# Performance work log

Measured on AMD Instinct MI355X. Metric: run time of the kernel, lower is better.

## Reference

```python
import jax, jax.numpy as jnp
import numpy as np

B, S, D, H = 2, 2048, 1024, 16
DK = D // H


def setup_inputs() -> dict:
    key = jax.random.key(0)
    ks = jax.random.split(key, 12)
    s = 0.02
    return {
        "q": jax.random.normal(ks[0], (B, S, D), jnp.float32),
        "k": jax.random.normal(ks[1], (B, S, D), jnp.float32),
        "v": jax.random.normal(ks[2], (B, S, D), jnp.float32),
        "mask": jax.random.randint(ks[3], (1, 1, S, S), 0, 2, jnp.int32),
        "Wq": jax.random.normal(ks[4], (D, D), jnp.float32) * s,
        "bq": jnp.zeros((D,), jnp.float32),
        "Wk": jax.random.normal(ks[5], (D, D), jnp.float32) * s,
        "bk": jnp.zeros((D,), jnp.float32),
        "Wv": jax.random.normal(ks[6], (D, D), jnp.float32) * s,
        "bv": jnp.zeros((D,), jnp.float32),
        "Wo": jax.random.normal(ks[7], (D, D), jnp.float32) * s,
        "bo": jnp.zeros((D,), jnp.float32),
    }


def reference(q, k, v, mask, Wq, bq, Wk, bk, Wv, bv, Wo, bo):
    # linear projections (torch Linear: x @ W.T + b)
    qp = q @ Wq.T + bq
    kp = k @ Wk.T + bk
    vp = v @ Wv.T + bv
    # [B, S, D] -> [B, H, S, DK]
    split = lambda x: x.reshape(B, S, H, DK).transpose(0, 2, 1, 3)
    qh, kh, vh = split(qp), split(kp), split(vp)
    scale = 1.0 / jnp.sqrt(jnp.float32(DK))
    attn = jnp.einsum('bhsd,bhtd->bhst', qh, kh) * scale  # [B,H,S,S]
    attn = jnp.where(mask == 0, jnp.float32(-1e9), attn)
    attn = jax.nn.softmax(attn, axis=-1)
    out = jnp.einsum('bhst,bhtd->bhsd', attn, vh)  # [B,H,S,DK]
    concat = out.transpose(0, 2, 1, 3).reshape(B, S, D)
    return concat @ Wo.T + bo
```

## Files before the change

kernel.cpp:

```cpp
#include <hip/hip_runtime.h>
#include <hip/hip_bf16.h>


using bf16x8 = __attribute__((ext_vector_type(8))) short;
using f32x4  = __attribute__((ext_vector_type(4))) float;

constexpr int Bc = 2, Sc = 2048, Dc = 1024, Hc = 16, DKc = 64;
constexpr int Mc = Bc * Sc;
#define QSCALE 0.18033688011112042f

__device__ __forceinline__ void lds_load16(const void* g, void* l) {
  __builtin_amdgcn_global_load_lds(
      (const __attribute__((address_space(1))) unsigned int*)g,
      (__attribute__((address_space(3))) unsigned int*)l, 16, 0, 0);
}

#if __has_builtin(__builtin_amdgcn_exp2f)
__device__ __forceinline__ float exp2_fast(float x) { return __builtin_amdgcn_exp2f(x); }
#else
__device__ __forceinline__ float exp2_fast(float x) {
  float r;
  asm("v_exp_f32 %0, %1\n\ts_nop 0" : "=v"(r) : "v"(x));
  return r;
}
#endif

__device__ __forceinline__ unsigned pack_trunc(float a, float b) {
  return __builtin_amdgcn_perm(__float_as_uint(b), __float_as_uint(a), 0x07060302u);
}

__device__ __forceinline__ unsigned pack2bf(float a, float b) {
  union { __hip_bfloat16 h; unsigned short s; } ua, ub;
  ua.h = __float2bfloat16(a);
  ub.h = __float2bfloat16(b);
  return (unsigned)ua.s | ((unsigned)ub.s << 16);
}

__global__ void prep(const float* __restrict__ q, const float* __restrict__ k,
                     const float* __restrict__ v, const int* __restrict__ mask,
                     const float* __restrict__ Wq, const float* __restrict__ Wk,
                     const float* __restrict__ Wv, const float* __restrict__ Wo,
                     char* __restrict__ ws) {
  const size_t MB = 1024 * 1024;
  int blk = blockIdx.x;
  if (blk < 12288) {
    int which = blk >> 12;
    int i = (((blk & 4095) << 8) + threadIdx.x) * 4;
    const float* s = which == 0 ? q : (which == 1 ? k : v);
    __hip_bfloat16* d = (__hip_bfloat16*)(ws + (size_t)which * 8 * MB);
    float4 x = *(const float4*)&s[i];
    uint2 pk = {pack2bf(x.x, x.y), pack2bf(x.z, x.w)};
    *(uint2*)&d[i] = pk;
  } else if (blk < 16384) {
    int bb = blk - 12288;
    int which = bb >> 10;
    int i = (((bb & 1023) << 8) + threadIdx.x) * 4;
    const float* s = which == 0 ? Wq : (which == 1 ? Wk : (which == 2 ? Wv : Wo));
    __hip_bfloat16* d = which < 3 ? (__hip_bfloat16*)(ws + (24 + 2 * which) * MB)
                                  : (__hip_bfloat16*)(ws + 30 * MB);
    float4 x = *(const float4*)&s[i];
    uint2 pk = {pack2bf(x.x, x.y), pack2bf(x.z, x.w)};
    *(uint2*)&d[i] = pk;
  } else {
    int i = ((blk - 16384) << 8) + threadIdx.x;
    unsigned long long bal = __ballot(mask[i] != 0);
    if ((threadIdx.x & 63) == 0)
      ((unsigned long long*)(ws + 32 * MB))[i >> 6] = bal;
  }
}

__global__ __launch_bounds__(256, 3) void proj_qkv(
    const __hip_bfloat16* __restrict__ qb, const __hip_bfloat16* __restrict__ kb,
    const __hip_bfloat16* __restrict__ vb, const __hip_bfloat16* __restrict__ Wcat,
    const float* __restrict__ bq, const float* __restrict__ bk,
    const float* __restrict__ bv, __hip_bfloat16* __restrict__ qhd,
    __hip_bfloat16* __restrict__ khd, __hip_bfloat16* __restrict__ vtd) {
  __shared__ __align__(16) __hip_bfloat16 As[2][128 * 32];
  __shared__ __align__(16) __hip_bfloat16 Bs[2][128 * 32];
  const int tid = threadIdx.x;
  const int f = blockIdx.x, g = f >> 3;
  const int m0 = ((f & 7) * 4 + g / 24) * 128;
  const int n0 = (g % 24) * 128;
  const int which = n0 >> 10, nl0 = n0 & 1023;
  const __hip_bfloat16* X = which == 0 ? qb : (which == 1 ? kb : vb);
  const float* bias = which == 0 ? bq : (which == 1 ? bk : bv);
  const int w = tid >> 6, lane = tid & 63, ln = lane & 15, quad = lane >> 4;
  const int rl = w * 32 + (lane >> 2);
  const int sw8 = ((lane & 3) ^ ((lane >> 2) & 3)) * 8;
  const int aoff = (n0 + rl) * 1024 + sw8;
  const int boff = (m0 + rl) * 1024 + sw8;
  char* aDst = (char*)As + w * 2048 + lane * 16;
  char* bDst = (char*)Bs + w * 2048 + lane * 16;
  const int rkq = (quad ^ (ln & 3)) * 16;
  const int rA0 = ((w >> 1) * 64 + ln) * 64 + rkq;
  const int rB0 = ((w & 1) * 64 + ln) * 64 + rkq;
  f32x4 acc[4][4] = {};

#define PSTAGE(KO, BI)                                                        \
  {                                                                           \
    lds_load16(&Wcat[aoff + (KO)], aDst + (BI)*8192);                         \
    lds_load16(&Wcat[aoff + 16384 + (KO)], aDst + (BI)*8192 + 1024);          \
    lds_load16(&X[boff + (KO)], bDst + (BI)*8192);                            \
    lds_load16(&X[boff + 16384 + (KO)], bDst + (BI)*8192 + 1024);             \
  }

  PSTAGE(0, 0);
  if (which == 2) {
    for (int kb32 = 0; kb32 < 32; ++kb32) {
      const int bi = kb32 & 1;
      __syncthreads();
      if (kb32 < 31) PSTAGE((kb32 + 1) * 32, bi ^ 1);
      bf16x8 af[4], bf[4];
#pragma unroll
      for (int i = 0; i < 4; ++i)
        af[i] = *(bf16x8*)((char*)As + bi * 8192 + rA0 + i * 1024);
#pragma unroll
      for (int j = 0; j < 4; ++j)
        bf[j] = *(bf16x8*)((char*)Bs + bi * 8192 + rB0 + j * 1024);
#pragma unroll
      for (int i = 0; i < 4; ++i)
#pragma unroll
        for (int j = 0; j < 4; ++j)
          acc[i][j] = __builtin_amdgcn_mfma_f32_16x16x32_bf16(bf[j], af[i],
                                                              acc[i][j], 0, 0, 0);
    }
  } else {
    for (int kb32 = 0; kb32 < 32; ++kb32) {
      const int bi = kb32 & 1;
      __syncthreads();
      if (kb32 < 31) PSTAGE((kb32 + 1) * 32, bi ^ 1);
      bf16x8 af[4], bf[4];
#pragma unroll
      for (int i = 0; i < 4; ++i)
        af[i] = *(bf16x8*)((char*)As + bi * 8192 + rA0 + i * 1024);
#pragma unroll
      for (int j = 0; j < 4; ++j)
        bf[j] = *(bf16x8*)((char*)Bs + bi * 8192 + rB0 + j * 1024);
#pragma unroll
      for (int i = 0; i < 4; ++i)
#pragma unroll
        for (int j = 0; j < 4; ++j)
          acc[i][j] = __builtin_amdgcn_mfma_f32_16x16x32_bf16(af[i], bf[j],
                                                              acc[i][j], 0, 0, 0);
    }
  }

  const int wA = (w >> 1) * 64, wB = (w & 1) * 64;
  if (which == 2) {
#pragma unroll
    for (int i = 0; i < 4; ++i) {
      int nf = nl0 + wA + i * 16 + ln;
      int h = nf >> 6, dk = nf & 63;
      float bb = bias[nf];
#pragma unroll
      for (int j = 0; j < 4; ++j) {
        int sb = m0 + wB + j * 16 + quad * 4;
        int b = sb >> 11, s = sb & 2047;
        float vv[4] = {acc[i][j][0] + bb, acc[i][j][1] + bb,
                       acc[i][j][2] + bb, acc[i][j][3] + bb};
        uint2 pk = {pack2bf(vv[0], vv[1]), pack2bf(vv[2], vv[3])};
        *(uint2*)&vtd[(((size_t)(b * Hc + h) * DKc + dk) * Sc) + s] = pk;
      }
    }
  } else {
#pragma unroll
    for (int i = 0; i < 4; ++i) {
      int nfb = nl0 + wA + i * 16 + quad * 4;
      float4 b4 = *(const float4*)&bias[nfb];
      int h = nfb >> 6, dk0 = nfb & 63;
#pragma unroll
      for (int j = 0; j < 4; ++j) {
        int sg = m0 + wB + j * 16 + ln;
        int b = sg >> 11, s = sg & 2047;
        float vv[4] = {acc[i][j][0] + b4.x, acc[i][j][1] + b4.y,
                       acc[i][j][2] + b4.z, acc[i][j][3] + b4.w};
        if (which == 0) {
          uint2 pk = {pack2bf(vv[0] * QSCALE, vv[1] * QSCALE),
                      pack2bf(vv[2] * QSCALE, vv[3] * QSCALE)};
          *(uint2*)&qhd[(((size_t)(b * Hc + h) * Sc + s) * DKc) + dk0] = pk;
        } else {
          uint2 pk = {pack2bf(vv[0], vv[1]), pack2bf(vv[2], vv[3])};
          *(uint2*)&khd[(((size_t)(b * Hc + h) * Sc + s) * DKc) + dk0] = pk;
        }
      }
    }
  }
}

__global__ __launch_bounds__(256, 2) void gemm_out(
    const __hip_bfloat16* __restrict__ X, const __hip_bfloat16* __restrict__ W,
    const float* __restrict__ bias, float* __restrict__ Y) {
  __shared__ __align__(16) __hip_bfloat16 As[2][64 * 64];
  __shared__ __align__(16) __hip_bfloat16 Bs[2][128 * 64];
  const int tid = threadIdx.x;
  const int f = blockIdx.x, g = f >> 3;
  const int m0 = ((f & 7) * 4 + (g >> 4)) * 128;
  const int n0 = (g & 15) * 64;
  const int w = tid >> 6, lane = tid & 63, ln = lane & 15, quad = lane >> 4;
  const int wA = (w & 1) * 32, wB = (w >> 1) * 64;
  const int swz = ((lane & 7) ^ (lane >> 3)) * 8;
  const int rk0 = ln * 128 + ((quad ^ (ln & 7)) * 16);
  const int rk1 = ln * 128 + (((quad + 4) ^ (ln & 7)) * 16);
  const int aoff = (n0 + w * 16 + (lane >> 3)) * 1024 + swz;
  const int boff = (m0 + w * 32 + (lane >> 3)) * 1024 + swz;
  f32x4 acc[2][4] = {};

#define OSTAGE(KO, BI)                                                        \
  {                                                                           \
    _Pragma("unroll") for (int i = 0; i < 2; ++i)                             \
        lds_load16(&W[aoff + i * 8192 + (KO)],                                \
                   (char*)As[BI] + w * 2048 + lane * 16 + i * 1024);          \
    _Pragma("unroll") for (int i = 0; i < 4; ++i)                             \
        lds_load16(&X[boff + i * 8192 + (KO)],                                \
                   (char*)Bs[BI] + w * 4096 + lane * 16 + i * 1024);          \
  }

  OSTAGE(0, 0);
  for (int kb64 = 0; kb64 < 16; ++kb64) {
    const int bi = kb64 & 1;
    __syncthreads();
    if (kb64 + 1 < 16) OSTAGE((kb64 + 1) * 64, bi ^ 1);
    bf16x8 af[2][2], bf[4][2];
#pragma unroll
    for (int i = 0; i < 2; ++i) {
      af[i][0] = *(bf16x8*)((char*)As[bi] + wA * 128 + i * 2048 + rk0);
      af[i][1] = *(bf16x8*)((char*)As[bi] + wA * 128 + i * 2048 + rk1);
    }
#pragma unroll
    for (int j = 0; j < 4; ++j) {
      bf[j][0] = *(bf16x8*)((char*)Bs[bi] + wB * 128 + j * 2048 + rk0);
      bf[j][1] = *(bf16x8*)((char*)Bs[bi] + wB * 128 + j * 2048 + rk1);
    }
#pragma unroll
    for (int i = 0; i < 2; ++i)
#pragma unroll
      for (int j = 0; j < 4; ++j) {
        acc[i][j] = __builtin_amdgcn_mfma_f32_16x16x32_bf16(af[i][0], bf[j][0],
                                                            acc[i][j], 0, 0, 0);
        acc[i][j] = __builtin_amdgcn_mfma_f32_16x16x32_bf16(af[i][1], bf[j][1],
                                                            acc[i][j], 0, 0, 0);
      }
  }
#pragma unroll
  for (int i = 0; i < 2; ++i) {
    int nfb = n0 + wA + i * 16 + quad * 4;
    float4 b4 = *(const float4*)&bias[nfb];
#pragma unroll
    for (int j = 0; j < 4; ++j) {
      int sg = m0 + wB + j * 16 + ln;
      float4 st = {acc[i][j][0] + b4.x, acc[i][j][1] + b4.y,
                   acc[i][j][2] + b4.z, acc[i][j][3] + b4.w};
      *(float4*)&Y[(size_t)sg * Dc + nfb] = st;
    }
  }
}

__global__ __launch_bounds__(256, 3) void flash_attn(
    const __hip_bfloat16* __restrict__ qh, const __hip_bfloat16* __restrict__ kh,
    const __hip_bfloat16* __restrict__ vt, const uint4* __restrict__ mb4,
    __hip_bfloat16* __restrict__ oc) {
  __shared__ __align__(16) char L[51200];
  const int tid = threadIdx.x;
  const int f = blockIdx.x, g = f >> 3;
  const int bh = (f & 7) * 4 + (g >> 4);
  const int q0 = (g & 15) * 128;
  const int b = bh >> 4, h = bh & 15;
  const int w = tid >> 6, lane = tid & 63, ln = lane & 15, quad = lane >> 4;
  const size_t base = (size_t)bh * Sc * DKc;
  const __hip_bfloat16* khb = kh + base;
  const __hip_bfloat16* vtb = vt + base;

  bf16x8 qf[2][2];
#pragma unroll
  for (int qt = 0; qt < 2; ++qt)
#pragma unroll
    for (int kc = 0; kc < 2; ++kc)
      qf[qt][kc] = *(const bf16x8*)&qh[base +
          (size_t)(q0 + w * 32 + qt * 16 + ln) * 64 + kc * 32 + quad * 8];

  bf16x8 onesA;
#pragma unroll
  for (int i = 0; i < 8; ++i) onesA[i] = (short)0x3F80;

  const int swz = ((lane & 7) ^ (lane >> 3)) * 8;
  const int rk0 = ln * 128 + ((quad ^ (ln & 7)) * 16);
  const int rk1 = ln * 128 + (((quad + 4) ^ (ln & 7)) * 16);
  const int rPw = 32768 + w * 4608 + ln * 144 + quad * 8;
  const int rPb = 32768 + w * 4608 + ln * 144 + quad * 16;
  char* dmaL = L + w * 2048 + lane * 16;
  int koff = (w * 16 + (lane >> 3)) * 64 + swz;
  int voff0 = (w * 16 + (lane >> 3)) * Sc + swz;
  int voff1 = voff0 + 8 * Sc;
  int midx0 = (q0 + w * 32 + ln) * 16;
  int midx1 = midx0 + 256;
  const int sh0 = quad * 4, sh1 = quad * 4 + 16;

#define KV_DMA(BI)                                                            \
  {                                                                           \
    lds_load16(khb + koff, dmaL + (BI)*8192);                                 \
    lds_load16(khb + koff + 512, dmaL + (BI)*8192 + 1024);                    \
    lds_load16(vtb + voff0, dmaL + 16384 + (BI)*8192);                        \
    lds_load16(vtb + voff1, dmaL + 16384 + (BI)*8192 + 1024);                 \
  }

  f32x4 Oacc[4][2] = {};
  f32x4 lacc[2] = {};
  KV_DMA(0);

#define FTILE(BUF, LO0, HI0, LO1, HI1)                                        \
  {                                                                           \
    bf16x8 kf[4][2];                                                          \
    _Pragma("unroll") for (int tt = 0; tt < 4; ++tt) {                        \
      kf[tt][0] = *(bf16x8*)(L + (BUF)*8192 + tt * 2048 + rk0);               \
      kf[tt][1] = *(bf16x8*)(L + (BUF)*8192 + tt * 2048 + rk1);               \
    }                                                                         \
    _Pragma("unroll") for (int qt = 0; qt < 2; ++qt) {                        \
      f32x4 s[4];                                                             \
      __builtin_amdgcn_s_setprio(1);                                          \
      _Pragma("unroll") for (int tt = 0; tt < 4; ++tt) {                      \
        f32x4 z = {0.f, 0.f, 0.f, 0.f};                                       \
        z = __builtin_amdgcn_mfma_f32_16x16x32_bf16(kf[tt][0], qf[qt][0], z,  \
                                                    0, 0, 0);                 \
        s[tt] = __builtin_amdgcn_mfma_f32_16x16x32_bf16(kf[tt][1], qf[qt][1], \
                                                        z, 0, 0, 0);          \
      }                                                                       \
      __builtin_amdgcn_s_setprio(0);                                          \
      unsigned lo = qt ? (LO1) : (LO0), hi = qt ? (HI1) : (HI0);              \
      _Pragma("unroll") for (int tt = 0; tt < 4; ++tt) {                      \
        unsigned word = (tt & 2) ? hi : lo;                                   \
        unsigned pre = word >> ((tt & 1) ? sh1 : sh0);                        \
        float p[4];                                                           \
        _Pragma("unroll") for (int r = 0; r < 4; ++r) {                       \
          float e = exp2_fast(s[tt][r]);                                      \
          p[r] = (pre & (1u << r)) ? e : 0.f;                                 \
        }                                                                     \
        uint2 pk = {pack_trunc(p[0], p[1]), pack_trunc(p[2], p[3])};          \
        *(uint2*)(L + rPw + qt * 2304 + tt * 32) = pk;                        \
      }                                                                       \
    }                                                                         \
    bf16x8 vf[4][2], pb[2][2];                                                \
    _Pragma("unroll") for (int dt = 0; dt < 4; ++dt) {                        \
      vf[dt][0] = *(bf16x8*)(L + 16384 + (BUF)*8192 + dt * 2048 + rk0);       \
      vf[dt][1] = *(bf16x8*)(L + 16384 + (BUF)*8192 + dt * 2048 + rk1);       \
    }                                                                         \
    _Pragma("unroll") for (int qt = 0; qt < 2; ++qt) {                        \
      pb[qt][0] = *(bf16x8*)(L + rPb + qt * 2304);                            \
      pb[qt][1] = *(bf16x8*)(L + rPb + qt * 2304 + 64);                       \
    }                                                                         \
    __builtin_amdgcn_s_setprio(1);                                            \
    _Pragma("unroll") for (int qt = 0; qt < 2; ++qt) {                        \
      lacc[qt] = __builtin_amdgcn_mfma_f32_16x16x32_bf16(onesA, pb[qt][0],    \
                                                         lacc[qt], 0, 0, 0);  \
      lacc[qt] = __builtin_amdgcn_mfma_f32_16x16x32_bf16(onesA, pb[qt][1],    \
                                                         lacc[qt], 0, 0, 0);  \
    }                                                                         \
    _Pragma("unroll") for (int dt = 0; dt < 4; ++dt)                          \
        _Pragma("unroll") for (int qt = 0; qt < 2; ++qt) {                    \
      Oacc[dt][qt] = __builtin_amdgcn_mfma_f32_16x16x32_bf16(                 \
          vf[dt][0], pb[qt][0], Oacc[dt][qt], 0, 0, 0);                       \
      Oacc[dt][qt] = __builtin_amdgcn_mfma_f32_16x16x32_bf16(                 \
          vf[dt][1], pb[qt][1], Oacc[dt][qt], 0, 0, 0);                       \
    }                                                                         \
    __builtin_amdgcn_s_setprio(0);                                            \
  }

  for (int it2 = 0; it2 < 16; ++it2) {
    __syncthreads();
    uint4 mq0 = mb4[midx0], mq1 = mb4[midx1];
    ++midx0; ++midx1;
    koff += 4096; voff0 += 64; voff1 += 64;
    KV_DMA(1);
    FTILE(0, mq0.x, mq0.y, mq1.x, mq1.y);
    __syncthreads();
    if (it2 < 15) {
      koff += 4096; voff0 += 64; voff1 += 64;
      KV_DMA(0);
    }
    FTILE(1, mq0.z, mq0.w, mq1.z, mq1.w);
  }

  float linv[2];
#pragma unroll
  for (int qt = 0; qt < 2; ++qt)
    linv[qt] = 1.f / fmaxf(lacc[qt][0], 1e-30f);
#pragma unroll
  for (int dt = 0; dt < 4; ++dt)
#pragma unroll
    for (int qt = 0; qt < 2; ++qt) {
      f32x4 o = Oacc[dt][qt];
      uint2 pk = {pack2bf(o[0] * linv[qt], o[1] * linv[qt]),
                  pack2bf(o[2] * linv[qt], o[3] * linv[qt])};
      *(uint2*)(L + rPw + qt * 2304 + dt * 32) = pk;
    }
  __builtin_amdgcn_s_waitcnt(0);
#pragma unroll
  for (int chunk = 0; chunk < 4; ++chunk) {
    int row = chunk * 8 + (lane >> 3);
    bf16x8 val = *(bf16x8*)(L + 32768 + w * 4608 + row * 144 + (lane & 7) * 16);
    int s = q0 + w * 32 + row;
    *(bf16x8*)&oc[(size_t)(b * Sc + s) * Dc + h * 64 + (lane & 7) * 8] = val;
  }
}

extern "C" void kernel_launch(void* const* d_in, const int* in_sizes, int n_in,
                              void* d_out, int out_size, void* d_ws, size_t ws_size,
                              hipStream_t stream) {
  const float* q  = (const float*)d_in[0];
  const float* k  = (const float*)d_in[1];
  const float* v  = (const float*)d_in[2];
  const int* mask = (const int*)d_in[3];
  const float* Wq = (const float*)d_in[4];
  const float* bq = (const float*)d_in[5];
  const float* Wk = (const float*)d_in[6];
  const float* bk = (const float*)d_in[7];
  const float* Wv = (const float*)d_in[8];
  const float* bv = (const float*)d_in[9];
  const float* Wo = (const float*)d_in[10];
  const float* bo = (const float*)d_in[11];

  char* ws = (char*)d_ws;
  const size_t MB = 1024 * 1024;
  __hip_bfloat16* qb   = (__hip_bfloat16*)(ws + 0 * MB);
  __hip_bfloat16* kb   = (__hip_bfloat16*)(ws + 8 * MB);
  __hip_bfloat16* vb   = (__hip_bfloat16*)(ws + 16 * MB);
  __hip_bfloat16* Wcat = (__hip_bfloat16*)(ws + 24 * MB);
  __hip_bfloat16* Wob  = (__hip_bfloat16*)(ws + 30 * MB);
  uint4*          mb4  = (uint4*)(ws + 32 * MB);
  __hip_bfloat16* qhd  = (__hip_bfloat16*)(ws + 33 * MB);
  __hip_bfloat16* khd  = (__hip_bfloat16*)(ws + 41 * MB);
  __hip_bfloat16* vtd  = (__hip_bfloat16*)(ws + 49 * MB);
  __hip_bfloat16* oc   = (__hip_bfloat16*)(ws + 57 * MB);

  prep<<<32768, 256, 0, stream>>>(q, k, v, mask, Wq, Wk, Wv, Wo, ws);
  proj_qkv<<<768, 256, 0, stream>>>(qb, kb, vb, Wcat, bq, bk, bv, qhd, khd, vtd);
  flash_attn<<<512, 256, 0, stream>>>(qhd, khd, vtd, mb4, oc);
  gemm_out<<<512, 256, 0, stream>>>(oc, Wob, bo, (float*)d_out);
}
```

Measured before the change: 241.4 us.

## Split flash-attention KV tiles across two wave groups with LDS reduction

Doubles the flash_attn block to 512 threads. Each pair of waves shares a 32-row query slice and splits every 64-key tile into two halves, so each wave does half the QK, softmax and PV work per tile. The partial O accumulators and row sums are combined through LDS at the end before the output is written. This raises per-CU wave parallelism to hide latency, at the cost of a final reduction, extra barriers, and tighter occupancy limits under launch_bounds(512,4).

```diff
diff --git a/kernel.cpp b/kernel.cpp
--- a/kernel.cpp
+++ b/kernel.cpp
@@ -255,7 +255,7 @@
   }
 }
 
-__global__ __launch_bounds__(256, 3) void flash_attn(
+__global__ __launch_bounds__(512, 4) void flash_attn(
     const __hip_bfloat16* __restrict__ qh, const __hip_bfloat16* __restrict__ kh,
     const __hip_bfloat16* __restrict__ vt, const uint4* __restrict__ mb4,
     __hip_bfloat16* __restrict__ oc) {
@@ -266,6 +266,7 @@
   const int q0 = (g & 15) * 128;
   const int b = bh >> 4, h = bh & 15;
   const int w = tid >> 6, lane = tid & 63, ln = lane & 15, quad = lane >> 4;
+  const int qg = w >> 1, kg = w & 1;
   const size_t base = (size_t)bh * Sc * DKc;
   const __hip_bfloat16* khb = kh + base;
   const __hip_bfloat16* vtb = vt + base;
@@ -276,7 +277,7 @@
 #pragma unroll
     for (int kc = 0; kc < 2; ++kc)
       qf[qt][kc] = *(const bf16x8*)&qh[base +
-          (size_t)(q0 + w * 32 + qt * 16 + ln) * 64 + kc * 32 + quad * 8];
+          (size_t)(q0 + qg * 32 + qt * 16 + ln) * 64 + kc * 32 + quad * 8];
 
   bf16x8 onesA;
 #pragma unroll
@@ -285,82 +286,69 @@
   const int swz = ((lane & 7) ^ (lane >> 3)) * 8;
   const int rk0 = ln * 128 + ((quad ^ (ln & 7)) * 16);
   const int rk1 = ln * 128 + (((quad + 4) ^ (ln & 7)) * 16);
-  const int rPw = 32768 + w * 4608 + ln * 144 + quad * 8;
-  const int rPb = 32768 + w * 4608 + ln * 144 + quad * 16;
-  char* dmaL = L + w * 2048 + lane * 16;
-  int koff = (w * 16 + (lane >> 3)) * 64 + swz;
-  int voff0 = (w * 16 + (lane >> 3)) * Sc + swz;
-  int voff1 = voff0 + 8 * Sc;
-  int midx0 = (q0 + w * 32 + ln) * 16;
+  const int rkv = ln * 128 + ((((kg << 2) + quad) ^ (ln & 7)) * 16);
+  const int rPw = 32768 + qg * 4608 + ln * 144 + kg * 64 + quad * 8;
+  const int rPb = 32768 + qg * 4608 + ln * 144 + kg * 64 + quad * 16;
+  char* dmaL = L + w * 1024 + lane * 16;
+  int koff = (w * 8 + (lane >> 3)) * 64 + swz;
+  int voff = (w * 8 + (lane >> 3)) * Sc + swz;
+  int midx0 = (q0 + qg * 32 + ln) * 16;
   int midx1 = midx0 + 256;
   const int sh0 = quad * 4, sh1 = quad * 4 + 16;
 
 #define KV_DMA(BI)                                                            \
   {                                                                           \
     lds_load16(khb + koff, dmaL + (BI)*8192);                                 \
-    lds_load16(khb + koff + 512, dmaL + (BI)*8192 + 1024);                    \
-    lds_load16(vtb + voff0, dmaL + 16384 + (BI)*8192);                        \
-    lds_load16(vtb + voff1, dmaL + 16384 + (BI)*8192 + 1024);                 \
+    lds_load16(vtb + voff, dmaL + 16384 + (BI)*8192);                         \
   }
 
   f32x4 Oacc[4][2] = {};
   f32x4 lacc[2] = {};
   KV_DMA(0);
 
-#define FTILE(BUF, LO0, HI0, LO1, HI1)                                        \
+#define FTILE(BUF, E0, E1)                                                    \
   {                                                                           \
-    bf16x8 kf[4][2];                                                          \
-    _Pragma("unroll") for (int tt = 0; tt < 4; ++tt) {                        \
-      kf[tt][0] = *(bf16x8*)(L + (BUF)*8192 + tt * 2048 + rk0);               \
-      kf[tt][1] = *(bf16x8*)(L + (BUF)*8192 + tt * 2048 + rk1);               \
+    bf16x8 kf[2][2];                                                          \
+    _Pragma("unroll") for (int tl = 0; tl < 2; ++tl) {                        \
+      kf[tl][0] = *(bf16x8*)(L + (BUF)*8192 + (kg * 2 + tl) * 2048 + rk0);    \
+      kf[tl][1] = *(bf16x8*)(L + (BUF)*8192 + (kg * 2 + tl) * 2048 + rk1);    \
     }                                                                         \
     _Pragma("unroll") for (int qt = 0; qt < 2; ++qt) {                        \
-      f32x4 s[4];                                                             \
+      f32x4 s4[2];                                                            \
       __builtin_amdgcn_s_setprio(1);                                          \
-      _Pragma("unroll") for (int tt = 0; tt < 4; ++tt) {                      \
+      _Pragma("unroll") for (int tl = 0; tl < 2; ++tl) {                      \
         f32x4 z = {0.f, 0.f, 0.f, 0.f};                                       \
-        z = __builtin_amdgcn_mfma_f32_16x16x32_bf16(kf[tt][0], qf[qt][0], z,  \
+        z = __builtin_amdgcn_mfma_f32_16x16x32_bf16(kf[tl][0], qf[qt][0], z,  \
                                                     0, 0, 0);                 \
-        s[tt] = __builtin_amdgcn_mfma_f32_16x16x32_bf16(kf[tt][1], qf[qt][1], \
-                                                        z, 0, 0, 0);          \
+        s4[tl] = __builtin_amdgcn_mfma_f32_16x16x32_bf16(kf[tl][1],           \
+                                                         qf[qt][1], z, 0, 0, 0); \
       }                                                                       \
       __builtin_amdgcn_s_setprio(0);                                          \
-      unsigned lo = qt ? (LO1) : (LO0), hi = qt ? (HI1) : (HI0);              \
-      _Pragma("unroll") for (int tt = 0; tt < 4; ++tt) {                      \
-        unsigned word = (tt & 2) ? hi : lo;                                   \
-        unsigned pre = word >> ((tt & 1) ? sh1 : sh0);                        \
+      unsigned word = qt ? (E1) : (E0);                                       \
+      _Pragma("unroll") for (int tl = 0; tl < 2; ++tl) {                      \
+        unsigned pre = word >> (tl ? sh1 : sh0);                              \
         float p[4];                                                           \
         _Pragma("unroll") for (int r = 0; r < 4; ++r) {                       \
-          float e = exp2_fast(s[tt][r]);                                      \
+          float e = exp2_fast(s4[tl][r]);                                     \
           p[r] = (pre & (1u << r)) ? e : 0.f;                                 \
         }                                                                     \
         uint2 pk = {pack_trunc(p[0], p[1]), pack_trunc(p[2], p[3])};          \
-        *(uint2*)(L + rPw + qt * 2304 + tt * 32) = pk;                        \
+        *(uint2*)(L + rPw + qt * 2304 + tl * 32) = pk;                        \
       }                                                                       \
     }                                                                         \
-    bf16x8 vf[4][2], pb[2][2];                                                \
-    _Pragma("unroll") for (int dt = 0; dt < 4; ++dt) {                        \
-      vf[dt][0] = *(bf16x8*)(L + 16384 + (BUF)*8192 + dt * 2048 + rk0);       \
-      vf[dt][1] = *(bf16x8*)(L + 16384 + (BUF)*8192 + dt * 2048 + rk1);       \
-    }                                                                         \
-    _Pragma("unroll") for (int qt = 0; qt < 2; ++qt) {                        \
-      pb[qt][0] = *(bf16x8*)(L + rPb + qt * 2304);                            \
-      pb[qt][1] = *(bf16x8*)(L + rPb + qt * 2304 + 64);                       \
-    }                                                                         \
+    bf16x8 vf[4], pb[2];                                                      \
+    _Pragma("unroll") for (int dt = 0; dt < 4; ++dt)                          \
+        vf[dt] = *(bf16x8*)(L + 16384 + (BUF)*8192 + dt * 2048 + rkv);        \
+    _Pragma("unroll") for (int qt = 0; qt < 2; ++qt)                          \
+        pb[qt] = *(bf16x8*)(L + rPb + qt * 2304);                             \
     __builtin_amdgcn_s_setprio(1);                                            \
-    _Pragma("unroll") for (int qt = 0; qt < 2; ++qt) {                        \
-      lacc[qt] = __builtin_amdgcn_mfma_f32_16x16x32_bf16(onesA, pb[qt][0],    \
-                                                         lacc[qt], 0, 0, 0);  \
-      lacc[qt] = __builtin_amdgcn_mfma_f32_16x16x32_bf16(onesA, pb[qt][1],    \
-                                                         lacc[qt], 0, 0, 0);  \
-    }                                                                         \
+    _Pragma("unroll") for (int qt = 0; qt < 2; ++qt)                          \
+        lacc[qt] = __builtin_amdgcn_mfma_f32_16x16x32_bf16(onesA, pb[qt],     \
+                                                           lacc[qt], 0, 0, 0); \
     _Pragma("unroll") for (int dt = 0; dt < 4; ++dt)                          \
-        _Pragma("unroll") for (int qt = 0; qt < 2; ++qt) {                    \
-      Oacc[dt][qt] = __builtin_amdgcn_mfma_f32_16x16x32_bf16(                 \
-          vf[dt][0], pb[qt][0], Oacc[dt][qt], 0, 0, 0);                       \
-      Oacc[dt][qt] = __builtin_amdgcn_mfma_f32_16x16x32_bf16(                 \
-          vf[dt][1], pb[qt][1], Oacc[dt][qt], 0, 0, 0);                       \
-    }                                                                         \
+        _Pragma("unroll") for (int qt = 0; qt < 2; ++qt)                      \
+            Oacc[dt][qt] = __builtin_amdgcn_mfma_f32_16x16x32_bf16(           \
+                vf[dt], pb[qt], Oacc[dt][qt], 0, 0, 0);                       \
     __builtin_amdgcn_s_setprio(0);                                            \
   }
 
@@ -368,38 +356,66 @@
     __syncthreads();
     uint4 mq0 = mb4[midx0], mq1 = mb4[midx1];
     ++midx0; ++midx1;
-    koff += 4096; voff0 += 64; voff1 += 64;
+    koff += 4096; voff += 64;
     KV_DMA(1);
-    FTILE(0, mq0.x, mq0.y, mq1.x, mq1.y);
+    FTILE(0, kg ? mq0.y : mq0.x, kg ? mq1.y : mq1.x);
     __syncthreads();
     if (it2 < 15) {
-      koff += 4096; voff0 += 64; voff1 += 64;
+      koff += 4096; voff += 64;
       KV_DMA(0);
     }
-    FTILE(1, mq0.z, mq0.w, mq1.z, mq1.w);
-  }
-
-  float linv[2];
-#pragma unroll
-  for (int qt = 0; qt < 2; ++qt)
-    linv[qt] = 1.f / fmaxf(lacc[qt][0], 1e-30f);
-#pragma unroll
-  for (int dt = 0; dt < 4; ++dt)
+    FTILE(1, kg ? mq0.w : mq0.z, kg ? mq1.w : mq1.z);
+  }
+
+  __syncthreads();
+  if (kg) {
+#pragma unroll
+    for (int dt = 0; dt < 4; ++dt)
+#pragma unroll
+      for (int qt = 0; qt < 2; ++qt) {
+        int slot = (dt * 4 + quad) ^ ln;
+        *(f32x4*)(L + qg * 8192 + (qt * 16 + ln) * 256 + slot * 16) =
+            Oacc[dt][qt];
+      }
+    if (quad == 0) {
+      *(float*)(L + 32768 + qg * 4608 + ln * 144 + 128) = lacc[0][0];
+      *(float*)(L + 32768 + qg * 4608 + 2304 + ln * 144 + 128) = lacc[1][0];
+    }
+  }
+  __syncthreads();
+  if (!kg) {
+    float linv[2];
 #pragma unroll
     for (int qt = 0; qt < 2; ++qt) {
-      f32x4 o = Oacc[dt][qt];
-      uint2 pk = {pack2bf(o[0] * linv[qt], o[1] * linv[qt]),
-                  pack2bf(o[2] * linv[qt], o[3] * linv[qt])};
-      *(uint2*)(L + rPw + qt * 2304 + dt * 32) = pk;
-    }
-  __builtin_amdgcn_s_waitcnt(0);
-#pragma unroll
-  for (int chunk = 0; chunk < 4; ++chunk) {
-    int row = chunk * 8 + (lane >> 3);
-    bf16x8 val = *(bf16x8*)(L + 32768 + w * 4608 + row * 144 + (lane & 7) * 16);
-    int s = q0 + w * 32 + row;
-    *(bf16x8*)&oc[(size_t)(b * Sc + s) * Dc + h * 64 + (lane & 7) * 8] = val;
-  }
+      float lsum = lacc[qt][0] +
+                   *(float*)(L + 32768 + qg * 4608 + qt * 2304 + ln * 144 + 128);
+      linv[qt] = 1.f / fmaxf(lsum, 1e-30f);
+    }
+#pragma unroll
+    for (int dt = 0; dt < 4; ++dt)
+#pragma unroll
+      for (int qt = 0; qt < 2; ++qt) {
+        int slot = (dt * 4 + quad) ^ ln;
+        f32x4 part =
+            *(f32x4*)(L + qg * 8192 + (qt * 16 + ln) * 256 + slot * 16);
+        f32x4 o = Oacc[dt][qt];
+        o[0] += part[0]; o[1] += part[1]; o[2] += part[2]; o[3] += part[3];
+        uint2 pk = {pack2bf(o[0] * linv[qt], o[1] * linv[qt]),
+                    pack2bf(o[2] * linv[qt], o[3] * linv[qt])};
+        *(uint2*)(L + rPw + qt * 2304 + dt * 32) = pk;
+      }
+    __builtin_amdgcn_s_waitcnt(0);
+#pragma unroll
+    for (int chunk = 0; chunk < 4; ++chunk) {
+      int row = chunk * 8 + (lane >> 3);
+      bf16x8 val =
+          *(bf16x8*)(L + 32768 + qg * 4608 + row * 144 + (lane & 7) * 16);
+      int s = q0 + qg * 32 + row;
+      *(bf16x8*)&oc[(size_t)(b * Sc + s) * Dc + h * 64 + (lane & 7) * 8] = val;
+    }
+  }
+#undef KV_DMA
+#undef FTILE
 }
 
 extern "C" void kernel_launch(void* const* d_in, const int* in_sizes, int n_in,
@@ -433,6 +449,6 @@
 
   prep<<<32768, 256, 0, stream>>>(q, k, v, mask, Wq, Wk, Wv, Wo, ws);
   proj_qkv<<<768, 256, 0, stream>>>(qb, kb, vb, Wcat, bq, bk, bv, qhd, khd, vtd);
-  flash_attn<<<512, 256, 0, stream>>>(qhd, khd, vtd, mb4, oc);
+  flash_attn<<<512, 512, 0, stream>>>(qhd, khd, vtd, mb4, oc);
   gemm_out<<<512, 256, 0, stream>>>(oc, Wob, bo, (float*)d_out);
 }
```

After: 244.7 us. Within noise of the previous version (+1.4%).

## Rewrite flash attention with 32x32x16 MFMA and register-resident P via permlane swap

Applied to the files above, without the earlier changes.

The attention kernel switches from 16x16x32 to 32x32x16 bf16 MFMA tiles. Softmax probabilities are packed with v_cvt_pk_bf16 and rearranged across lanes with v_permlane32_swap, so they stay in registers instead of round-tripping through LDS, and LDS use drops to 32KB. It also reads the mask as uint2 per tile, writes output directly from registers, and lowers the launch-bounds occupancy hint from 3 to 2. The aim is fewer LDS transactions and MFMA instructions per tile, traded against more registers per thread and a mask layout that must match what prep writes, which is not visible here.

```diff
diff --git a/kernel.cpp b/kernel.cpp
--- a/kernel.cpp
+++ b/kernel.cpp
@@ -4,6 +4,7 @@
 
 using bf16x8 = __attribute__((ext_vector_type(8))) short;
 using f32x4  = __attribute__((ext_vector_type(4))) float;
+using f32x16 = __attribute__((ext_vector_type(16))) float;
 
 constexpr int Bc = 2, Sc = 2048, Dc = 1024, Hc = 16, DKc = 64;
 constexpr int Mc = Bc * Sc;
@@ -25,9 +26,14 @@
 }
 #endif
 
-__device__ __forceinline__ unsigned pack_trunc(float a, float b) {
-  return __builtin_amdgcn_perm(__float_as_uint(b), __float_as_uint(a), 0x07060302u);
-}
+__device__ __forceinline__ unsigned cvt_pk_bf16(float lo, float hi) {
+  unsigned r;
+  asm("v_cvt_pk_bf16_f32 %0, %1, %2" : "=v"(r) : "v"(lo), "v"(hi));
+  return r;
+}
+
+#define PSWAP(A, B) \
+  asm volatile("v_permlane32_swap_b32 %0, %1" : "+v"(A), "+v"(B))
 
 __device__ __forceinline__ unsigned pack2bf(float a, float b) {
   union { __hip_bfloat16 h; unsigned short s; } ua, ub;
@@ -255,151 +261,126 @@
   }
 }
 
-__global__ __launch_bounds__(256, 3) void flash_attn(
+__global__ __launch_bounds__(256, 2) void flash_attn(
     const __hip_bfloat16* __restrict__ qh, const __hip_bfloat16* __restrict__ kh,
-    const __hip_bfloat16* __restrict__ vt, const uint4* __restrict__ mb4,
+    const __hip_bfloat16* __restrict__ vt, const uint2* __restrict__ mb2,
     __hip_bfloat16* __restrict__ oc) {
-  __shared__ __align__(16) char L[51200];
+  __shared__ __align__(16) char L[32768];
   const int tid = threadIdx.x;
   const int f = blockIdx.x, g = f >> 3;
   const int bh = (f & 7) * 4 + (g >> 4);
   const int q0 = (g & 15) * 128;
   const int b = bh >> 4, h = bh & 15;
-  const int w = tid >> 6, lane = tid & 63, ln = lane & 15, quad = lane >> 4;
+  const int w = tid >> 6, lane = tid & 63, l31 = lane & 31, hi = lane >> 5;
   const size_t base = (size_t)bh * Sc * DKc;
   const __hip_bfloat16* khb = kh + base;
   const __hip_bfloat16* vtb = vt + base;
-
-  bf16x8 qf[2][2];
-#pragma unroll
-  for (int qt = 0; qt < 2; ++qt)
-#pragma unroll
-    for (int kc = 0; kc < 2; ++kc)
-      qf[qt][kc] = *(const bf16x8*)&qh[base +
-          (size_t)(q0 + w * 32 + qt * 16 + ln) * 64 + kc * 32 + quad * 8];
+  const int qglob = q0 + w * 32 + l31;
+
+  bf16x8 qf[4];
+#pragma unroll
+  for (int dt = 0; dt < 4; ++dt)
+    qf[dt] = *(const bf16x8*)&qh[base + (size_t)qglob * 64 + dt * 16 + hi * 8];
 
   bf16x8 onesA;
 #pragma unroll
   for (int i = 0; i < 8; ++i) onesA[i] = (short)0x3F80;
 
-  const int swz = ((lane & 7) ^ (lane >> 3)) * 8;
-  const int rk0 = ln * 128 + ((quad ^ (ln & 7)) * 16);
-  const int rk1 = ln * 128 + (((quad + 4) ^ (ln & 7)) * 16);
-  const int rPw = 32768 + w * 4608 + ln * 144 + quad * 8;
-  const int rPb = 32768 + w * 4608 + ln * 144 + quad * 16;
-  char* dmaL = L + w * 2048 + lane * 16;
-  int koff = (w * 16 + (lane >> 3)) * 64 + swz;
-  int voff0 = (w * 16 + (lane >> 3)) * Sc + swz;
-  int voff1 = voff0 + 8 * Sc;
-  int midx0 = (q0 + w * 32 + ln) * 16;
-  int midx1 = midx0 + 256;
-  const int sh0 = quad * 4, sh1 = quad * 4 + 16;
-
-#define KV_DMA(BI)                                                            \
+  const int trow = tid >> 3, tcol = tid & 7;
+  const int kbase = trow * 64 + ((tcol ^ (trow & 7)) * 8);
+  const int vbase = trow * 2048 + ((tcol ^ (trow & 7)) * 8);
+  char* Ld = L + tid * 16;
+
+  const int rowb = l31 * 128;
+  const int xs = lane & 7;
+
+  f32x16 Oacc0 = {}, Oacc1 = {}, lacc = {};
+
+#define STAGE(BI, T)                                                          \
   {                                                                           \
-    lds_load16(khb + koff, dmaL + (BI)*8192);                                 \
-    lds_load16(khb + koff + 512, dmaL + (BI)*8192 + 1024);                    \
-    lds_load16(vtb + voff0, dmaL + 16384 + (BI)*8192);                        \
-    lds_load16(vtb + voff1, dmaL + 16384 + (BI)*8192 + 1024);                 \
-  }
-
-  f32x4 Oacc[4][2] = {};
-  f32x4 lacc[2] = {};
-  KV_DMA(0);
-
-#define FTILE(BUF, LO0, HI0, LO1, HI1)                                        \
+    lds_load16(khb + kbase + (T)*4096,        Ld + (BI)*8192);                \
+    lds_load16(khb + kbase + (T)*4096 + 2048, Ld + (BI)*8192 + 4096);         \
+    lds_load16(vtb + vbase + (T)*64,          Ld + 16384 + (BI)*8192);        \
+    lds_load16(vtb + vbase + (T)*64 + 65536,  Ld + 16384 + (BI)*8192 + 4096); \
+  }
+
+#define PROC_SUB(BOFF, SUB, MW)                                               \
   {                                                                           \
-    bf16x8 kf[4][2];                                                          \
-    _Pragma("unroll") for (int tt = 0; tt < 4; ++tt) {                        \
-      kf[tt][0] = *(bf16x8*)(L + (BUF)*8192 + tt * 2048 + rk0);               \
-      kf[tt][1] = *(bf16x8*)(L + (BUF)*8192 + tt * 2048 + rk1);               \
+    bf16x8 kf0 = *(bf16x8*)(L + (BOFF) + (SUB)*4096 + rowb + (((0 + hi) ^ xs) * 16)); \
+    bf16x8 kf1 = *(bf16x8*)(L + (BOFF) + (SUB)*4096 + rowb + (((2 + hi) ^ xs) * 16)); \
+    bf16x8 kf2 = *(bf16x8*)(L + (BOFF) + (SUB)*4096 + rowb + (((4 + hi) ^ xs) * 16)); \
+    bf16x8 kf3 = *(bf16x8*)(L + (BOFF) + (SUB)*4096 + rowb + (((6 + hi) ^ xs) * 16)); \
+    f32x16 c = {};                                                            \
+    __builtin_amdgcn_s_setprio(1);                                            \
+    c = __builtin_amdgcn_mfma_f32_32x32x16_bf16(kf0, qf[0], c, 0, 0, 0);      \
+    c = __builtin_amdgcn_mfma_f32_32x32x16_bf16(kf1, qf[1], c, 0, 0, 0);      \
+    c = __builtin_amdgcn_mfma_f32_32x32x16_bf16(kf2, qf[2], c, 0, 0, 0);      \
+    c = __builtin_amdgcn_mfma_f32_32x32x16_bf16(kf3, qf[3], c, 0, 0, 0);      \
+    __builtin_amdgcn_s_setprio(0);                                            \
+    unsigned shm = (MW) >> (hi * 4);                                          \
+    float p[16];                                                              \
+    _Pragma("unroll") for (int r = 0; r < 16; ++r) {                          \
+      unsigned tg = shm >> (8 * (r >> 2));                                    \
+      float e = exp2_fast(c[r]);                                              \
+      p[r] = (tg & (1u << (r & 3))) ? e : 0.f;                                \
     }                                                                         \
-    _Pragma("unroll") for (int qt = 0; qt < 2; ++qt) {                        \
-      f32x4 s[4];                                                             \
-      __builtin_amdgcn_s_setprio(1);                                          \
-      _Pragma("unroll") for (int tt = 0; tt < 4; ++tt) {                      \
-        f32x4 z = {0.f, 0.f, 0.f, 0.f};                                       \
-        z = __builtin_amdgcn_mfma_f32_16x16x32_bf16(kf[tt][0], qf[qt][0], z,  \
-                                                    0, 0, 0);                 \
-        s[tt] = __builtin_amdgcn_mfma_f32_16x16x32_bf16(kf[tt][1], qf[qt][1], \
-                                                        z, 0, 0, 0);          \
-      }                                                                       \
-      __builtin_amdgcn_s_setprio(0);                                          \
-      unsigned lo = qt ? (LO1) : (LO0), hi = qt ? (HI1) : (HI0);              \
-      _Pragma("unroll") for (int tt = 0; tt < 4; ++tt) {                      \
-        unsigned word = (tt & 2) ? hi : lo;                                   \
-        unsigned pre = word >> ((tt & 1) ? sh1 : sh0);                        \
-        float p[4];                                                           \
-        _Pragma("unroll") for (int r = 0; r < 4; ++r) {                       \
-          float e = exp2_fast(s[tt][r]);                                      \
-          p[r] = (pre & (1u << r)) ? e : 0.f;                                 \
-        }                                                                     \
-        uint2 pk = {pack_trunc(p[0], p[1]), pack_trunc(p[2], p[3])};          \
-        *(uint2*)(L + rPw + qt * 2304 + tt * 32) = pk;                        \
-      }                                                                       \
-    }                                                                         \
-    bf16x8 vf[4][2], pb[2][2];                                                \
-    _Pragma("unroll") for (int dt = 0; dt < 4; ++dt) {                        \
-      vf[dt][0] = *(bf16x8*)(L + 16384 + (BUF)*8192 + dt * 2048 + rk0);       \
-      vf[dt][1] = *(bf16x8*)(L + 16384 + (BUF)*8192 + dt * 2048 + rk1);       \
-    }                                                                         \
-    _Pragma("unroll") for (int qt = 0; qt < 2; ++qt) {                        \
-      pb[qt][0] = *(bf16x8*)(L + rPb + qt * 2304);                            \
-      pb[qt][1] = *(bf16x8*)(L + rPb + qt * 2304 + 64);                       \
-    }                                                                         \
-    __builtin_amdgcn_s_setprio(1);                                            \
-    _Pragma("unroll") for (int qt = 0; qt < 2; ++qt) {                        \
-      lacc[qt] = __builtin_amdgcn_mfma_f32_16x16x32_bf16(onesA, pb[qt][0],    \
-                                                         lacc[qt], 0, 0, 0);  \
-      lacc[qt] = __builtin_amdgcn_mfma_f32_16x16x32_bf16(onesA, pb[qt][1],    \
-                                                         lacc[qt], 0, 0, 0);  \
-    }                                                                         \
-    _Pragma("unroll") for (int dt = 0; dt < 4; ++dt)                          \
-        _Pragma("unroll") for (int qt = 0; qt < 2; ++qt) {                    \
-      Oacc[dt][qt] = __builtin_amdgcn_mfma_f32_16x16x32_bf16(                 \
-          vf[dt][0], pb[qt][0], Oacc[dt][qt], 0, 0, 0);                       \
-      Oacc[dt][qt] = __builtin_amdgcn_mfma_f32_16x16x32_bf16(                 \
-          vf[dt][1], pb[qt][1], Oacc[dt][qt], 0, 0, 0);                       \
-    }                                                                         \
-    __builtin_amdgcn_s_setprio(0);                                            \
-  }
-
-  for (int it2 = 0; it2 < 16; ++it2) {
+    unsigned w0 = cvt_pk_bf16(p[0], p[1]),   w1 = cvt_pk_bf16(p[2], p[3]);    \
+    unsigned w2 = cvt_pk_bf16(p[4], p[5]),   w3 = cvt_pk_bf16(p[6], p[7]);    \
+    unsigned w4 = cvt_pk_bf16(p[8], p[9]),   w5 = cvt_pk_bf16(p[10], p[11]);  \
+    unsigned w6 = cvt_pk_bf16(p[12], p[13]), w7 = cvt_pk_bf16(p[14], p[15]);  \
+    PSWAP(w0, w2); PSWAP(w1, w3); PSWAP(w4, w6); PSWAP(w5, w7);               \
+    { union { unsigned u[4]; bf16x8 v; } t;                                   \
+      t.u[0] = w0; t.u[1] = w1; t.u[2] = w2; t.u[3] = w3;                     \
+      pb[(SUB)*2] = t.v; }                                                    \
+    { union { unsigned u[4]; bf16x8 v; } t;                                   \
+      t.u[0] = w4; t.u[1] = w5; t.u[2] = w6; t.u[3] = w7;                     \
+      pb[(SUB)*2 + 1] = t.v; }                                                \
+  }
+
+  const uint2* mrow = mb2 + (size_t)qglob * 32;
+  uint2 mbC = mrow[0];
+  STAGE(0, 0);
+
+  for (int t = 0; t < 32; ++t) {
     __syncthreads();
-    uint4 mq0 = mb4[midx0], mq1 = mb4[midx1];
-    ++midx0; ++midx1;
-    koff += 4096; voff0 += 64; voff1 += 64;
-    KV_DMA(1);
-    FTILE(0, mq0.x, mq0.y, mq1.x, mq1.y);
-    __syncthreads();
-    if (it2 < 15) {
-      koff += 4096; voff0 += 64; voff1 += 64;
-      KV_DMA(0);
-    }
-    FTILE(1, mq0.z, mq0.w, mq1.z, mq1.w);
-  }
-
-  float linv[2];
-#pragma unroll
-  for (int qt = 0; qt < 2; ++qt)
-    linv[qt] = 1.f / fmaxf(lacc[qt][0], 1e-30f);
-#pragma unroll
-  for (int dt = 0; dt < 4; ++dt)
-#pragma unroll
-    for (int qt = 0; qt < 2; ++qt) {
-      f32x4 o = Oacc[dt][qt];
-      uint2 pk = {pack2bf(o[0] * linv[qt], o[1] * linv[qt]),
-                  pack2bf(o[2] * linv[qt], o[3] * linv[qt])};
-      *(uint2*)(L + rPw + qt * 2304 + dt * 32) = pk;
-    }
-  __builtin_amdgcn_s_waitcnt(0);
-#pragma unroll
-  for (int chunk = 0; chunk < 4; ++chunk) {
-    int row = chunk * 8 + (lane >> 3);
-    bf16x8 val = *(bf16x8*)(L + 32768 + w * 4608 + row * 144 + (lane & 7) * 16);
-    int s = q0 + w * 32 + row;
-    *(bf16x8*)&oc[(size_t)(b * Sc + s) * Dc + h * 64 + (lane & 7) * 8] = val;
-  }
+    uint2 mbN = mbC;
+    if (t < 31) {
+      mbN = mrow[t + 1];
+      STAGE((t + 1) & 1, t + 1);
+    }
+    const int boff = (t & 1) * 8192;
+
+    bf16x8 pb[4];
+    PROC_SUB(boff, 0, mbC.x);
+    PROC_SUB(boff, 1, mbC.y);
+
+    __builtin_amdgcn_s_setprio(1);
+#pragma unroll
+    for (int kt = 0; kt < 4; ++kt) {
+      lacc = __builtin_amdgcn_mfma_f32_32x32x16_bf16(onesA, pb[kt], lacc, 0, 0, 0);
+      bf16x8 vf0 = *(bf16x8*)(L + 16384 + boff + rowb + (((kt * 2 + hi) ^ xs) * 16));
+      bf16x8 vf1 = *(bf16x8*)(L + 16384 + boff + 4096 + rowb + (((kt * 2 + hi) ^ xs) * 16));
+      Oacc0 = __builtin_amdgcn_mfma_f32_32x32x16_bf16(vf0, pb[kt], Oacc0, 0, 0, 0);
+      Oacc1 = __builtin_amdgcn_mfma_f32_32x32x16_bf16(vf1, pb[kt], Oacc1, 0, 0, 0);
+    }
+    __builtin_amdgcn_s_setprio(0);
+    mbC = mbN;
+  }
+
+  float linv = 1.f / fmaxf(lacc[0], 1e-30f);
+  const size_t obase = (size_t)(b * Sc + qglob) * Dc + h * 64;
+#pragma unroll
+  for (int gq = 0; gq < 4; ++gq) {
+    int d0 = gq * 8 + hi * 4;
+    uint2 pk0 = {pack2bf(Oacc0[4 * gq] * linv, Oacc0[4 * gq + 1] * linv),
+                 pack2bf(Oacc0[4 * gq + 2] * linv, Oacc0[4 * gq + 3] * linv)};
+    *(uint2*)&oc[obase + d0] = pk0;
+    uint2 pk1 = {pack2bf(Oacc1[4 * gq] * linv, Oacc1[4 * gq + 1] * linv),
+                 pack2bf(Oacc1[4 * gq + 2] * linv, Oacc1[4 * gq + 3] * linv)};
+    *(uint2*)&oc[obase + 32 + d0] = pk1;
+  }
+#undef STAGE
+#undef PROC_SUB
 }
 
 extern "C" void kernel_launch(void* const* d_in, const int* in_sizes, int n_in,
@@ -425,7 +406,7 @@
   __hip_bfloat16* vb   = (__hip_bfloat16*)(ws + 16 * MB);
   __hip_bfloat16* Wcat = (__hip_bfloat16*)(ws + 24 * MB);
   __hip_bfloat16* Wob  = (__hip_bfloat16*)(ws + 30 * MB);
-  uint4*          mb4  = (uint4*)(ws + 32 * MB);
+  uint2*          mb2  = (uint2*)(ws + 32 * MB);
   __hip_bfloat16* qhd  = (__hip_bfloat16*)(ws + 33 * MB);
   __hip_bfloat16* khd  = (__hip_bfloat16*)(ws + 41 * MB);
   __hip_bfloat16* vtd  = (__hip_bfloat16*)(ws + 49 * MB);
@@ -433,6 +414,6 @@
 
   prep<<<32768, 256, 0, stream>>>(q, k, v, mask, Wq, Wk, Wv, Wo, ws);
   proj_qkv<<<768, 256, 0, stream>>>(qb, kb, vb, Wcat, bq, bk, bv, qhd, khd, vtd);
-  flash_attn<<<512, 256, 0, stream>>>(qhd, khd, vtd, mb4, oc);
+  flash_attn<<<512, 256, 0, stream>>>(qhd, khd, vtd, mb2, oc);
   gemm_out<<<512, 256, 0, stream>>>(oc, Wob, bo, (float*)d_out);
 }
```

New measurement: 243.8 us. No clear change (+1.0%).
